# Optimization experiments

Measured on AMD Instinct MI355X. Metric: run time of the kernel, lower is better.

Reference implementation:

```python
import jax, jax.numpy as jnp
import numpy as np

B, S, E = 2, 2048, 1024
H, D = 16, 64          # num_heads, head_dim
FF = 4096              # ff_dim = 4*E
EPS = 1e-5


def _layer_norm(x, g, b):
    mu = jnp.mean(x, axis=-1, keepdims=True)
    var = jnp.mean(jnp.square(x - mu), axis=-1, keepdims=True)
    return (x - mu) * jax.lax.rsqrt(var + EPS) * g + b


def setup_inputs() -> dict:
    key = jax.random.key(0)
    ks = jax.random.split(key, 9)
    s = lambda fan_in: 1.0 / np.sqrt(fan_in)
    return {
        "x": jax.random.normal(ks[0], (B, S, E), dtype=jnp.float32),
        "w_qkv": jax.random.uniform(ks[1], (3 * E, E), jnp.float32, -s(E), s(E)),
        "b_qkv": jnp.zeros((3 * E,), jnp.float32),
        "w_out": jax.random.uniform(ks[2], (E, E), jnp.float32, -s(E), s(E)),
        "b_out": jnp.zeros((E,), jnp.float32),
        "g1": jnp.ones((E,), jnp.float32),
        "beta1": jnp.zeros((E,), jnp.float32),
        "w_fc1": jax.random.uniform(ks[3], (FF, E), jnp.float32, -s(E), s(E)),
        "b_fc1": jnp.zeros((FF,), jnp.float32),
        "w_fc2": jax.random.uniform(ks[4], (E, FF), jnp.float32, -s(FF), s(FF)),
        "b_fc2": jnp.zeros((E,), jnp.float32),
        "g2": jnp.ones((E,), jnp.float32),
        "beta2": jnp.zeros((E,), jnp.float32),
    }


def reference(x, w_qkv, b_qkv, w_out, b_out, g1, beta1, w_fc1, b_fc1, w_fc2, b_fc2, g2, beta2):
    scale = 1.0 / np.sqrt(D)
    # QKV projection: [B,S,3E] -> [3,B,H,S,D]
    qkv = (x @ w_qkv.T + b_qkv).reshape(B, S, 3, H, D).transpose(2, 0, 3, 1, 4)
    q, k, v = qkv[0], qkv[1], qkv[2]
    attn = jax.nn.softmax(jnp.einsum('bhqd,bhkd->bhqk', q, k) * scale, axis=-1)
    out = jnp.einsum('bhqk,bhkd->bhqd', attn, v)          # [B,H,S,D]
    out = out.transpose(0, 2, 1, 3).reshape(B, S, E)
    attn_out = out @ w_out.T + b_out
    x1 = _layer_norm(x + attn_out, g1, beta1)
    h = jax.nn.gelu(x1 @ w_fc1.T + b_fc1, approximate=False)  # torch GELU = exact erf
    ff_out = h @ w_fc2.T + b_fc2
    return _layer_norm(x1 + ff_out, g2, beta2)
```

## Files before the change

### kernel.cpp

```cpp
#include <hip/hip_runtime.h>
#include <hip/hip_bf16.h>
#include <math.h>
#include <type_traits>

typedef __hip_bfloat16 bf16;
using short8  = __attribute__((ext_vector_type(8))) short;
using short4v = __attribute__((ext_vector_type(4))) short;
using f32x4   = __attribute__((ext_vector_type(4))) float;

#define TS 2048
#define TH 16
#define TD 64
#define TE 1024
#define T2E 2048

__device__ __forceinline__ void gload16(void* lds, const void* g) {
    __builtin_amdgcn_global_load_lds(
        (__attribute__((address_space(1))) void*)g,
        (__attribute__((address_space(3))) void*)lds, 16, 0, 0);
}

__device__ __forceinline__ uint32_t pktrunc(float a, float b) {
    return (__builtin_bit_cast(uint32_t, a) >> 16) |
           (__builtin_bit_cast(uint32_t, b) & 0xFFFF0000u);
}

__global__ __launch_bounds__(256) void f2b_multi(
    const float* __restrict__ s0, bf16* __restrict__ d0,
    const float* __restrict__ s1, bf16* __restrict__ d1,
    const float* __restrict__ s2, bf16* __restrict__ d2,
    const float* __restrict__ s3, bf16* __restrict__ d3,
    const float* __restrict__ s4, bf16* __restrict__ d4)
{
    int blk = blockIdx.x;
    const float* s; bf16* d; int base;
    if (blk < 2048)      { s = s0; d = d0; base = 0; }
    else if (blk < 3584) { s = s1; d = d1; base = 2048; }
    else if (blk < 4096) { s = s2; d = d2; base = 3584; }
    else if (blk < 6144) { s = s3; d = d3; base = 4096; }
    else                 { s = s4; d = d4; base = 6144; }
    size_t i = ((size_t)(blk - base) * 256 + threadIdx.x) * 8;
    float4 a = *(const float4*)&s[i];
    float4 b = *(const float4*)&s[i + 4];
    bf16 t[8];
    t[0] = __float2bfloat16(a.x); t[1] = __float2bfloat16(a.y);
    t[2] = __float2bfloat16(a.z); t[3] = __float2bfloat16(a.w);
    t[4] = __float2bfloat16(b.x); t[5] = __float2bfloat16(b.y);
    t[6] = __float2bfloat16(b.z); t[7] = __float2bfloat16(b.w);
    *(uint4*)&d[i] = *(uint4*)t;
}

template <typename TC, bool GELU, bool QS, bool WVT, int BN>
__global__ __launch_bounds__(512, 2) void gemm256(
    const bf16* __restrict__ A, const bf16* __restrict__ Bw,
    const float* __restrict__ bias, TC* __restrict__ C,
    bf16* __restrict__ vTout, int M, int N, int K, int kLen, int Cstride)
{
    constexpr int NB = BN / 64;
    constexpr int NI = BN / 64;
    constexpr int WN = BN / 4;
    __shared__ bf16 As[2][256 * 64];
    __shared__ bf16 Bs[2][BN * 64];

    const int t    = threadIdx.x;
    const int lane = t & 63;
    const int wv   = t >> 6;
    const int wr   = wv >> 2;
    const int wc   = wv & 3;
    const int lr   = lane & 15;
    const int lq   = lane >> 4;

    const int gx  = gridDim.x, gxy = gridDim.x * gridDim.y;
    const int nwg = gxy * gridDim.z;
    const int id  = blockIdx.x + gx * blockIdx.y + gxy * blockIdx.z;
    const int sid = (id & 7) * (nwg >> 3) + (id >> 3);
    const int zIdx  = sid / gxy;
    const int rem   = sid - zIdx * gxy;
    const int tm    = rem / gx;
    const int mBase = tm * 256;
    const int nBase = (rem - tm * gx) * BN;
    const int kOff  = zIdx * kLen;

    const int sr = t >> 3;
    const int sc = (((t & 7) ^ ((t >> 3) & 7)) * 8);
    const int NT = kLen >> 6;

    const bf16* aPt = A  + (size_t)(mBase + sr) * K + sc;
    const bf16* bPt = Bw + (size_t)(nBase + sr) * K + sc;

    f32x4 acc[8][NI];
    #pragma unroll
    for (int mi = 0; mi < 8; mi++)
        #pragma unroll
        for (int ni = 0; ni < NI; ni++)
            acc[mi][ni] = (f32x4){0.f, 0.f, 0.f, 0.f};

    auto stage = [&](int b, int k0) {
        #pragma unroll
        for (int i = 0; i < 4; i++)
            gload16(&As[b][i * 4096 + wv * 512],
                    aPt + (size_t)(i * 64) * K + k0);
        #pragma unroll
        for (int i = 0; i < NB; i++)
            gload16(&Bs[b][i * 4096 + wv * 512],
                    bPt + (size_t)(i * 64) * K + k0);
    };

    stage(0, kOff);
    for (int kt = 0; kt < NT; ++kt) {
        const int cur = kt & 1;
        if (kt + 1 < NT) {
            stage(cur ^ 1, kOff + (kt + 1) * 64);
            if constexpr (BN == 256)
                asm volatile("s_waitcnt vmcnt(8)" ::: "memory");
            else if constexpr (BN == 192)
                asm volatile("s_waitcnt vmcnt(7)" ::: "memory");
            else
                asm volatile("s_waitcnt vmcnt(6)" ::: "memory");
        } else {
            asm volatile("s_waitcnt vmcnt(0)" ::: "memory");
        }
        __builtin_amdgcn_s_barrier();
        asm volatile("" ::: "memory");

        short8 bfr[NI][2];
        #pragma unroll
        for (int ni = 0; ni < NI; ni++)
            #pragma unroll
            for (int ks = 0; ks < 2; ks++) {
                int row = wc * WN + ni * 16 + lr;
                int col = (ks * 32 + lq * 8) ^ ((lr & 7) * 8);
                bfr[ni][ks] = *(const short8*)&Bs[cur][row * 64 + col];
            }
        #pragma unroll
        for (int mi = 0; mi < 8; mi++) {
            int row = wr * 128 + mi * 16 + lr;
            int c0 = (lq * 8) ^ ((lr & 7) * 8);
            int c1 = (32 + lq * 8) ^ ((lr & 7) * 8);
            short8 a0 = *(const short8*)&As[cur][row * 64 + c0];
            short8 a1 = *(const short8*)&As[cur][row * 64 + c1];
            #pragma unroll
            for (int ni = 0; ni < NI; ni++) {
                acc[mi][ni] = __builtin_amdgcn_mfma_f32_16x16x32_bf16(
                    a0, bfr[ni][0], acc[mi][ni], 0, 0, 0);
                acc[mi][ni] = __builtin_amdgcn_mfma_f32_16x16x32_bf16(
                    a1, bfr[ni][1], acc[mi][ni], 0, 0, 0);
            }
        }
        asm volatile("s_waitcnt lgkmcnt(0)" ::: "memory");
        __builtin_amdgcn_s_barrier();
    }

    const size_t cOff = (size_t)zIdx * M * Cstride;
    #pragma unroll
    for (int mi = 0; mi < 8; mi++) {
        #pragma unroll
        for (int ni = 0; ni < NI; ni++) {
            int cc = nBase + wc * WN + ni * 16 + lr;
            float bv = (zIdx == 0) ? bias[cc] : 0.f;
            int r0 = mBase + wr * 128 + mi * 16 + lq * 4;
            bool vpath = false;
            if constexpr (WVT) {
                if (cc >= 2 * TE) {
                    vpath = true;
                    int d  = cc - 2 * TE;
                    int s0 = r0 & (TS - 1);
                    int bb = r0 >> 11;
                    int pos = (s0 & ~31) | (((s0 >> 2) & 3) << 3)
                            | (((s0 >> 4) & 1) << 2);
                    bf16 ob[4];
                    #pragma unroll
                    for (int i = 0; i < 4; i++)
                        ob[i] = __float2bfloat16(acc[mi][ni][i] + bv);
                    *(uint2*)&vTout[((size_t)(bb * TH + (d >> 6)) * TD + (d & 63))
                                    * TS + pos] = *(uint2*)ob;
                }
            }
            if (!vpath) {
                #pragma unroll
                for (int i = 0; i < 4; i++) {
                    float v = acc[mi][ni][i] + bv;
                    if constexpr (GELU)
                        v = 0.5f * v * (1.0f + erff(v * 0.70710678118f));
                    if constexpr (QS)
                        if (cc < TE) v *= 0.180336880111f;
                    if constexpr (std::is_same_v<TC, bf16>)
                        C[cOff + (size_t)(r0 + i) * Cstride + cc] = __float2bfloat16(v);
                    else
                        C[cOff + (size_t)(r0 + i) * Cstride + cc] = v;
                }
            }
        }
    }
}

__global__ __launch_bounds__(512, 2) void gemm128n(
    const bf16* __restrict__ A, const bf16* __restrict__ Bw,
    const float* __restrict__ bias, float* __restrict__ C,
    int M, int N, int K, int kLen)
{
    __shared__ bf16 As[3][128 * 64];
    __shared__ bf16 Bs[3][256 * 64];

    const int t    = threadIdx.x;
    const int lane = t & 63;
    const int wv   = t >> 6;
    const int wr   = wv >> 2;
    const int wc   = wv & 3;
    const int lr   = lane & 15;
    const int lq   = lane >> 4;

    const int gx  = gridDim.x, gxy = gridDim.x * gridDim.y;
    const int nwg = gxy * gridDim.z;
    const int id  = blockIdx.x + gx * blockIdx.y + gxy * blockIdx.z;
    const int sid = (id & 7) * (nwg >> 3) + (id >> 3);
    const int zIdx  = sid / gxy;
    const int rem   = sid - zIdx * gxy;
    const int tm    = rem / gx;
    const int mBase = tm * 128;
    const int nBase = (rem - tm * gx) * 256;
    const int kOff  = zIdx * kLen;

    const int sr = t >> 3;
    const int sc = (((t & 7) ^ ((t >> 3) & 7)) * 8);

    const bf16* aPt = A  + (size_t)(mBase + sr) * K + sc;
    const bf16* bPt = Bw + (size_t)(nBase + sr) * K + sc;

    f32x4 acc[4][4];
    #pragma unroll
    for (int mi = 0; mi < 4; mi++)
        #pragma unroll
        for (int ni = 0; ni < 4; ni++)
            acc[mi][ni] = (f32x4){0.f, 0.f, 0.f, 0.f};

    auto stage = [&](int b, int k0) {
        #pragma unroll
        for (int i = 0; i < 2; i++)
            gload16(&As[b][i * 4096 + wv * 512],
                    aPt + (size_t)(i * 64) * K + k0);
        #pragma unroll
        for (int i = 0; i < 4; i++)
            gload16(&Bs[b][i * 4096 + wv * 512],
                    bPt + (size_t)(i * 64) * K + k0);
    };

    const int NT = kLen >> 6;
    stage(0, kOff);
    stage(1, kOff + 64);
    int cur = 0;
    for (int kt = 0; kt < NT; ++kt) {
        if (kt + 2 < NT) {
            int nb = cur + 2; if (nb >= 3) nb -= 3;
            stage(nb, kOff + (kt + 2) * 64);
            asm volatile("s_waitcnt vmcnt(12)" ::: "memory");
        } else if (kt + 1 < NT) {
            asm volatile("s_waitcnt vmcnt(6)" ::: "memory");
        } else {
            asm volatile("s_waitcnt vmcnt(0)" ::: "memory");
        }
        __builtin_amdgcn_s_barrier();
        asm volatile("" ::: "memory");

        short8 af[4][2], bfr[4][2];
        #pragma unroll
        for (int mi = 0; mi < 4; mi++)
            #pragma unroll
            for (int ks = 0; ks < 2; ks++) {
                int row = wr * 64 + mi * 16 + lr;
                int col = (ks * 32 + lq * 8) ^ ((lr & 7) * 8);
                af[mi][ks] = *(const short8*)&As[cur][row * 64 + col];
            }
        #pragma unroll
        for (int ni = 0; ni < 4; ni++)
            #pragma unroll
            for (int ks = 0; ks < 2; ks++) {
                int row = wc * 64 + ni * 16 + lr;
                int col = (ks * 32 + lq * 8) ^ ((lr & 7) * 8);
                bfr[ni][ks] = *(const short8*)&Bs[cur][row * 64 + col];
            }
        #pragma unroll
        for (int mi = 0; mi < 4; mi++)
            #pragma unroll
            for (int ni = 0; ni < 4; ni++) {
                acc[mi][ni] = __builtin_amdgcn_mfma_f32_16x16x32_bf16(
                    af[mi][0], bfr[ni][0], acc[mi][ni], 0, 0, 0);
                acc[mi][ni] = __builtin_amdgcn_mfma_f32_16x16x32_bf16(
                    af[mi][1], bfr[ni][1], acc[mi][ni], 0, 0, 0);
            }
        asm volatile("s_waitcnt lgkmcnt(0)" ::: "memory");
        __builtin_amdgcn_s_barrier();
        cur += 1; if (cur >= 3) cur = 0;
    }

    const size_t cOff = (size_t)zIdx * M * N;
    #pragma unroll
    for (int mi = 0; mi < 4; mi++) {
        #pragma unroll
        for (int ni = 0; ni < 4; ni++) {
            int cc = nBase + wc * 64 + ni * 16 + lr;
            float bv = (zIdx == 0) ? bias[cc] : 0.f;
            int r0 = mBase + wr * 64 + mi * 16 + lq * 4;
            #pragma unroll
            for (int i = 0; i < 4; i++)
                C[cOff + (size_t)(r0 + i) * N + cc] = acc[mi][ni][i] + bv;
        }
    }
}

__global__ __launch_bounds__(256, 4) void attn_flash(
    const bf16* __restrict__ qkv, const bf16* __restrict__ vT,
    bf16* __restrict__ attnO)
{
    __shared__ bf16 Ks[128 * 72];
    __shared__ bf16 Vt[64 * 136];

    const int t    = threadIdx.x;
    const int lane = t & 63;
    const int wv   = t >> 6;
    const int c    = lane & 15;
    const int u    = lane >> 4;
    const int bid  = blockIdx.x;
    const int bh   = (bid & 7) * 4 + ((bid >> 3) & 3);
    const int qt   = bid >> 5;
    const int h = bh & 15, b = bh >> 4;
    const size_t tokBase = (size_t)b * TS;
    const int qrow = qt * 64 + wv * 16 + c;

    short8 qf[2];
    #pragma unroll
    for (int kc = 0; kc < 2; kc++)
        qf[kc] = *(const short8*)&qkv[(tokBase + qrow) * T2E + h * TD + kc * 32 + u * 8];

    f32x4 oacc[4];
    #pragma unroll
    for (int di = 0; di < 4; di++) oacc[di] = (f32x4){0.f, 0.f, 0.f, 0.f};
    float lsum = 0.f;

    const int vd = t >> 2;
    const int vc = (t & 3) * 8;
    const bf16* vbase = &vT[((size_t)bh * TD + vd) * TS + vc];

    for (int it = 0; it < 16; it++) {
        const int kb0 = it * 128;
        __syncthreads();

        #pragma unroll
        for (int i = 0; i < 4; i++) {
            int l = t + i * 256;
            int r = l >> 3, ch = (l & 7) * 8;
            *(uint4*)&Ks[r * 72 + ch] =
                *(const uint4*)&qkv[(tokBase + kb0 + r) * T2E + TE + h * TD + ch];
        }
        #pragma unroll
        for (int i = 0; i < 4; i++)
            *(uint4*)&Vt[vd * 136 + vc + i * 32] = *(const uint4*)&vbase[kb0 + i * 32];
        __syncthreads();

        f32x4 sacc[8];
        #pragma unroll
        for (int kc = 0; kc < 2; kc++) {
            #pragma unroll
            for (int kb = 0; kb < 8; kb++) {
                short8 kf = *(const short8*)&Ks[(kb * 16 + c) * 72 + kc * 32 + u * 8];
                sacc[kb] = __builtin_amdgcn_mfma_f32_16x16x32_bf16(
                    kf, qf[kc],
                    kc == 0 ? (f32x4){0.f, 0.f, 0.f, 0.f} : sacc[kb], 0, 0, 0);
            }
        }

        #pragma unroll
        for (int p = 0; p < 4; p++) {
            union { uint32_t d[2]; short4v s; } pb0, pb1;
            {
                float a0 = exp2f(sacc[2*p][0]);
                float a1 = exp2f(sacc[2*p][1]);
                float a2 = exp2f(sacc[2*p][2]);
                float a3 = exp2f(sacc[2*p][3]);
                float b0 = exp2f(sacc[2*p+1][0]);
                float b1 = exp2f(sacc[2*p+1][1]);
                float b2 = exp2f(sacc[2*p+1][2]);
                float b3 = exp2f(sacc[2*p+1][3]);
                lsum += (a0 + a1) + (a2 + a3) + (b0 + b1) + (b2 + b3);
                pb0.d[0] = pktrunc(a0, a1); pb0.d[1] = pktrunc(a2, a3);
                pb1.d[0] = pktrunc(b0, b1); pb1.d[1] = pktrunc(b2, b3);
            }
            #pragma unroll
            for (int di = 0; di < 4; di++) {
                short8 vv = *(const short8*)&Vt[(di * 16 + c) * 136 + p * 32 + u * 8];
                short4v lo = __builtin_shufflevector(vv, vv, 0, 1, 2, 3);
                short4v hi = __builtin_shufflevector(vv, vv, 4, 5, 6, 7);
                oacc[di] = __builtin_amdgcn_mfma_f32_16x16x16bf16_1k(
                    lo, pb0.s, oacc[di], 0, 0, 0);
                oacc[di] = __builtin_amdgcn_mfma_f32_16x16x16bf16_1k(
                    hi, pb1.s, oacc[di], 0, 0, 0);
            }
        }
    }

    lsum += __shfl_xor(lsum, 16, 64);
    lsum += __shfl_xor(lsum, 32, 64);
    const float inv = 1.0f / lsum;

    #pragma unroll
    for (int di = 0; di < 4; di++) {
        bf16 ob[4];
        #pragma unroll
        for (int rg = 0; rg < 4; rg++)
            ob[rg] = __float2bfloat16(oacc[di][rg] * inv);
        *(uint2*)&attnO[(tokBase + qrow) * TE + h * TD + di * 16 + u * 4] = *(uint2*)ob;
    }
}

__global__ __launch_bounds__(256) void add_ln3(
    const float* __restrict__ a, const float* __restrict__ p0,
    const float* __restrict__ p1, const float* __restrict__ g,
    const float* __restrict__ beta, float* __restrict__ out,
    bf16* __restrict__ outb)
{
    __shared__ float r1[256], r2[256];
    const int t = threadIdx.x;
    const size_t row = (size_t)blockIdx.x * TE;

    float4 va = *(const float4*)&a[row + t * 4];
    float4 v0 = *(const float4*)&p0[row + t * 4];
    float4 v1 = *(const float4*)&p1[row + t * 4];
    float v[4] = {va.x + v0.x + v1.x, va.y + v0.y + v1.y,
                  va.z + v0.z + v1.z, va.w + v0.w + v1.w};
    float s = 0.f, s2 = 0.f;
    #pragma unroll
    for (int i = 0; i < 4; i++) { s += v[i]; s2 += v[i] * v[i]; }
    r1[t] = s; r2[t] = s2;
    __syncthreads();
    for (int off = 128; off > 0; off >>= 1) {
        if (t < off) { r1[t] += r1[t + off]; r2[t] += r2[t + off]; }
        __syncthreads();
    }
    const float mu  = r1[0] * (1.f / 1024.f);
    const float var = r2[0] * (1.f / 1024.f) - mu * mu;
    const float rs  = rsqrtf(var + 1e-5f);
    float4 vg  = *(const float4*)&g[t * 4];
    float4 vbt = *(const float4*)&beta[t * 4];
    float o[4];
    o[0] = (v[0] - mu) * rs * vg.x + vbt.x;
    o[1] = (v[1] - mu) * rs * vg.y + vbt.y;
    o[2] = (v[2] - mu) * rs * vg.z + vbt.z;
    o[3] = (v[3] - mu) * rs * vg.w + vbt.w;
    *(float4*)&out[row + t * 4] = *(float4*)o;
    if (outb) {
        bf16 ob[4];
        #pragma unroll
        for (int i = 0; i < 4; i++) ob[i] = __float2bfloat16(o[i]);
        *(uint2*)&outb[row + t * 4] = *(uint2*)ob;
    }
}

extern "C" void kernel_launch(void* const* d_in, const int* in_sizes, int n_in,
                              void* d_out, int out_size, void* d_ws, size_t ws_size,
                              hipStream_t stream)
{
    const float* x     = (const float*)d_in[0];
    const float* w_qkv = (const float*)d_in[1];
    const float* b_qkv = (const float*)d_in[2];
    const float* w_out = (const float*)d_in[3];
    const float* b_out = (const float*)d_in[4];
    const float* g1    = (const float*)d_in[5];
    const float* beta1 = (const float*)d_in[6];
    const float* w_fc1 = (const float*)d_in[7];
    const float* b_fc1 = (const float*)d_in[8];
    const float* w_fc2 = (const float*)d_in[9];
    const float* b_fc2 = (const float*)d_in[10];
    const float* g2    = (const float*)d_in[11];
    const float* beta2 = (const float*)d_in[12];
    float* out = (float*)d_out;

    char* wsb   = (char*)d_ws;
    bf16*  qk    = (bf16*)(wsb);
    bf16*  vT    = (bf16*)(wsb + 16777216);
    bf16*  xb    = (bf16*)(wsb + 25165824);
    float* y     = (float*)(wsb);
    float* ff    = (float*)(wsb);
    bf16*  attnO = (bf16*)(wsb + 33554432);
    bf16*  x1b   = (bf16*)(wsb + 33554432);
    bf16*  wfc1b = (bf16*)(wsb + 41943040);
    bf16*  woutb = (bf16*)(wsb + 50331648);
    bf16*  wqkvb = (bf16*)(wsb + 52428800);
    float* x1    = (float*)(wsb + 67108864);
    bf16*  hbuf  = (bf16*)(wsb + 83886080);
    bf16*  wfc2b = (bf16*)(wsb + 117440512);

    const int M = 2 * TS;
    const size_t PART = (size_t)M * TE;
    dim3 blk(256), blk8(512);

    f2b_multi<<<dim3(8192), blk, 0, stream>>>(
        x, xb, w_qkv, wqkvb, w_out, woutb, w_fc1, wfc1b, w_fc2, wfc2b);

    gemm256<bf16, false, true, true, 192><<<dim3(16, 16, 1), blk8, 0, stream>>>(
        xb, wqkvb, b_qkv, qk, vT, M, 3072, TE, TE, T2E);
    attn_flash<<<dim3(1024), blk, 0, stream>>>(qk, vT, attnO);
    gemm128n<<<dim3(4, 32, 2), blk8, 0, stream>>>(
        attnO, woutb, b_out, y, M, TE, TE, TE / 2);
    add_ln3<<<dim3(M), blk, 0, stream>>>(x, y, y + PART, g1, beta1, x1, x1b);
    gemm256<bf16, true, false, false, 256><<<dim3(16, 16, 1), blk8, 0, stream>>>(
        x1b, wfc1b, b_fc1, hbuf, nullptr, M, 4096, TE, TE, 4096);
    gemm128n<<<dim3(4, 32, 2), blk8, 0, stream>>>(
        hbuf, wfc2b, b_fc2, ff, M, TE, 4096, 2048);
    add_ln3<<<dim3(M), blk, 0, stream>>>(x1, ff, ff + PART, g2, beta2, out, nullptr);
}
```

Baseline: 364.4 us.

## Halve attention key tile and use single 16x16x32 MFMA for PV

```diff
diff --git a/kernel.cpp b/kernel.cpp
--- a/kernel.cpp
+++ b/kernel.cpp
@@ -312,8 +312,8 @@
     const bf16* __restrict__ qkv, const bf16* __restrict__ vT,
     bf16* __restrict__ attnO)
 {
-    __shared__ bf16 Ks[128 * 72];
-    __shared__ bf16 Vt[64 * 136];
+    __shared__ bf16 Ks[64 * 72];
+    __shared__ bf16 Vt[64 * 72];
 
     const int t    = threadIdx.x;
     const int lane = t & 63;
@@ -337,31 +337,29 @@
     for (int di = 0; di < 4; di++) oacc[di] = (f32x4){0.f, 0.f, 0.f, 0.f};
     float lsum = 0.f;
 
-    const int vd = t >> 2;
-    const int vc = (t & 3) * 8;
-    const bf16* vbase = &vT[((size_t)bh * TD + vd) * TS + vc];
-
-    for (int it = 0; it < 16; it++) {
-        const int kb0 = it * 128;
+    const int kr  = t >> 3, kch = (t & 7) * 8;
+    const bf16* kbase = &qkv[(tokBase + kr) * T2E + TE + h * TD + kch];
+    const bf16* vbase = &vT[((size_t)bh * TD + kr) * TS + kch];
+
+    for (int it = 0; it < 32; it++) {
+        const int kb0 = it * 64;
         __syncthreads();
 
         #pragma unroll
-        for (int i = 0; i < 4; i++) {
-            int l = t + i * 256;
-            int r = l >> 3, ch = (l & 7) * 8;
-            *(uint4*)&Ks[r * 72 + ch] =
-                *(const uint4*)&qkv[(tokBase + kb0 + r) * T2E + TE + h * TD + ch];
-        }
-        #pragma unroll
-        for (int i = 0; i < 4; i++)
-            *(uint4*)&Vt[vd * 136 + vc + i * 32] = *(const uint4*)&vbase[kb0 + i * 32];
+        for (int i = 0; i < 2; i++)
+            *(uint4*)&Ks[(kr + i * 32) * 72 + kch] =
+                *(const uint4*)&kbase[(size_t)(kb0 + i * 32) * T2E];
+        #pragma unroll
+        for (int i = 0; i < 2; i++)
+            *(uint4*)&Vt[(kr + i * 32) * 72 + kch] =
+                *(const uint4*)&vbase[(size_t)(i * 32) * TS + kb0];
         __syncthreads();
 
-        f32x4 sacc[8];
+        f32x4 sacc[4];
         #pragma unroll
         for (int kc = 0; kc < 2; kc++) {
             #pragma unroll
-            for (int kb = 0; kb < 8; kb++) {
+            for (int kb = 0; kb < 4; kb++) {
                 short8 kf = *(const short8*)&Ks[(kb * 16 + c) * 72 + kc * 32 + u * 8];
                 sacc[kb] = __builtin_amdgcn_mfma_f32_16x16x32_bf16(
                     kf, qf[kc],
@@ -370,8 +368,8 @@
         }
 
         #pragma unroll
-        for (int p = 0; p < 4; p++) {
-            union { uint32_t d[2]; short4v s; } pb0, pb1;
+        for (int p = 0; p < 2; p++) {
+            union { uint32_t dd[4]; short8 s8; } pbc;
             {
                 float a0 = exp2f(sacc[2*p][0]);
                 float a1 = exp2f(sacc[2*p][1]);
@@ -382,18 +380,14 @@
                 float b2 = exp2f(sacc[2*p+1][2]);
                 float b3 = exp2f(sacc[2*p+1][3]);
                 lsum += (a0 + a1) + (a2 + a3) + (b0 + b1) + (b2 + b3);
-                pb0.d[0] = pktrunc(a0, a1); pb0.d[1] = pktrunc(a2, a3);
-                pb1.d[0] = pktrunc(b0, b1); pb1.d[1] = pktrunc(b2, b3);
+                pbc.dd[0] = pktrunc(a0, a1); pbc.dd[1] = pktrunc(a2, a3);
+                pbc.dd[2] = pktrunc(b0, b1); pbc.dd[3] = pktrunc(b2, b3);
             }
             #pragma unroll
             for (int di = 0; di < 4; di++) {
-                short8 vv = *(const short8*)&Vt[(di * 16 + c) * 136 + p * 32 + u * 8];
-                short4v lo = __builtin_shufflevector(vv, vv, 0, 1, 2, 3);
-                short4v hi = __builtin_shufflevector(vv, vv, 4, 5, 6, 7);
-                oacc[di] = __builtin_amdgcn_mfma_f32_16x16x16bf16_1k(
-                    lo, pb0.s, oacc[di], 0, 0, 0);
-                oacc[di] = __builtin_amdgcn_mfma_f32_16x16x16bf16_1k(
-                    hi, pb1.s, oacc[di], 0, 0, 0);
+                short8 vv = *(const short8*)&Vt[(di * 16 + c) * 72 + p * 32 + u * 8];
+                oacc[di] = __builtin_amdgcn_mfma_f32_16x16x32_bf16(
+                    vv, pbc.s8, oacc[di], 0, 0, 0);
             }
         }
     }
```

Result: no change. 368.2 us (+1.0%).
